# Kernel optimization log

Measured on AMD Instinct MI355X. Metric: run time of the kernel, lower is better.

## Reference

```python
import jax, jax.numpy as jnp
import numpy as np
from jax import lax

WINDOW_SIZE = 11
SIGMA = 1.5
MAX_VAL = 1.0
C1 = (MAX_VAL * 0.01) ** 2
C2 = (MAX_VAL * 0.03) ** 2


def _make_window(channel: int, k: int = WINDOW_SIZE, sigma: float = SIGMA) -> np.ndarray:
    x = np.arange(k, dtype=np.float64)
    g = np.exp(-((x - k // 2) ** 2) / (2.0 * sigma ** 2))
    g = (g / g.sum()).astype(np.float32)
    # rank-1 separable 3D window, built as dense [C,1,k,k,k] kernel (OIDHW, groups=C)
    w3 = g[:, None, None] * g[None, :, None] * g[None, None, :]
    return np.broadcast_to(w3, (channel, 1, k, k, k)).copy()


def _dwconv3d(x, kernel, pad):
    # depthwise 3D conv, SAME padding for odd kernel
    return lax.conv_general_dilated(
        x, kernel, window_strides=(1, 1, 1), padding=[(pad, pad)] * 3,
        dimension_numbers=("NCDHW", "OIDHW", "NCDHW"),
        feature_group_count=kernel.shape[0])


def setup_inputs() -> dict:
    key = jax.random.key(0)
    k1, k2 = jax.random.split(key)
    shape = (2, 4, 64, 160, 160)  # [B, C, D, H, W]
    img1 = jax.random.uniform(k1, shape, dtype=jnp.float32)
    img2 = jax.random.uniform(k2, shape, dtype=jnp.float32)
    return {"img1": img1, "img2": img2}


def reference(img1, img2):
    channel = img1.shape[1]
    window = jnp.asarray(_make_window(channel))
    pad = WINDOW_SIZE // 2
    # mask = ones_like(img1) in the original -> identity multiply, omitted
    mu1 = _dwconv3d(img1, window, pad)
    mu2 = _dwconv3d(img2, window, pad)
    mu1_sq = mu1 * mu1
    mu2_sq = mu2 * mu2
    mu1_mu2 = mu1 * mu2
    sigma1_sq = _dwconv3d(img1 * img1, window, pad) - mu1_sq
    sigma2_sq = _dwconv3d(img2 * img2, window, pad) - mu2_sq
    sigma12 = _dwconv3d(img1 * img2, window, pad) - mu1_mu2
    ssim_map = ((2.0 * mu1_mu2 + C1) * (2.0 * sigma12 + C2)) / (
        (mu1_sq + mu2_sq + C1) * (sigma1_sq + sigma2_sq + C2))
    ssim = jnp.mean(ssim_map, axis=(0, 2, 3, 4))  # per-channel SSIM, shape [C]
    return 1.0 - ssim
```

## Files before the change

### kernel.cpp

```cpp
#include <hip/hip_runtime.h>
#include <math.h>

typedef float v2f __attribute__((ext_vector_type(2)));

namespace {

constexpr int C_DIM = 4;
constexpr int D_DIM = 64;
constexpr int H_DIM = 160;
constexpr int W_DIM = 160;

constexpr int TH = 16;
constexpr int TW = 16;
constexpr int HALO = 5;
constexpr int EH = 26;
constexpr int EW = 26;
constexpr int XST = 27;
constexpr int MST = 17;
constexpr int NPIX = EH * EW;

constexpr int TILES_W = 10;
constexpr int TPC = 100;
constexpr int NBLOCKS = 2 * C_DIM * TPC;

constexpr float C1f = 1e-4f;
constexpr float C2f = 9e-4f;
constexpr float INV_N = 1.0f / (2.0f * 64.0f * 160.0f * 160.0f);

struct GW { float g[11]; };

}

__global__ void finalize_kernel(const float* __restrict__ partial,
                                float* __restrict__ out) {
    const int tid = threadIdx.x;
    const int c = tid >> 6;
    const int lane = tid & 63;
    float s = 0.0f;
#pragma unroll
    for (int b = 0; b < 2; ++b)
        for (int i = lane; i < TPC; i += 64)
            s += partial[b * (C_DIM * TPC) + c * TPC + i];
#pragma unroll
    for (int off = 32; off > 0; off >>= 1) s += __shfl_down(s, off, 64);
    if (lane == 0 && c < C_DIM) out[c] = 1.0f - s * INV_N;
}

__global__ __launch_bounds__(256, 4) void ssim3d_kernel(
    const float* __restrict__ img1, const float* __restrict__ img2,
    float* __restrict__ partial, GW gwp) {

    const int bid = blockIdx.x;
    const int tile = bid % TPC;
    const int c = (bid / TPC) % C_DIM;
    const int b = bid / (TPC * C_DIM);
    const int h0 = (tile / TILES_W) * TH;
    const int w0 = (tile % TILES_W) * TW;

    const long planeHW = (long)H_DIM * W_DIM;
    const long volbase = (long)(b * C_DIM + c) * D_DIM * planeHW;
    const long org = volbase + (long)(h0 - HALO) * W_DIM + (w0 - HALO);
    const float* __restrict__ p1 = img1 + org;
    const float* __restrict__ p2 = img2 + org;

    const bool interior = (h0 >= HALO) && (h0 + TH + HALO <= H_DIM) &&
                          (w0 >= HALO) && (w0 + TW + HALO <= W_DIM);

    __shared__ v2f    xy[2][EH][XST];
    __shared__ float4 mid[EH][MST];
    __shared__ float  rbuf[4];

    const int tid = threadIdx.x;

    int hh_[3], ww_[3], off_[3];
    bool live_[3], ok_[3];
#pragma unroll
    for (int k = 0; k < 3; ++k) {
        const int e = tid + k * 256;
        live_[k] = (e < NPIX);
        const int hh = e / EW;
        const int ww = e - hh * EW;
        hh_[k] = hh; ww_[k] = ww;
        off_[k] = hh * W_DIM + ww;
        const int gh = h0 - HALO + hh;
        const int gw = w0 - HALO + ww;
        ok_[k] = ((unsigned)gh < (unsigned)H_DIM) &&
                 ((unsigned)gw < (unsigned)W_DIM);
    }

    auto fetch_slice = [&](int s, v2f lv[3]) {
        const long sb = (long)s * planeHW;
#pragma unroll
        for (int k = 0; k < 3; ++k) {
            lv[k] = (v2f){0.0f, 0.0f};
            if (live_[k] && (interior || ok_[k])) {
                const long gi = sb + off_[k];
                lv[k].x = p1[gi];
                lv[k].y = p2[gi];
            }
        }
    };
    auto commit_slice = [&](int buf, const v2f lv[3]) {
#pragma unroll
        for (int k = 0; k < 3; ++k)
            if (live_[k]) xy[buf][hh_[k]][ww_[k]] = lv[k];
    };

    const bool wactive = (tid < 208);
    const int whh = tid % 26;
    const int wwg = (tid / 26) * 2;

    auto wconv = [&](int cur) {
        v2f a0 = {0.f, 0.f}, b0 = {0.f, 0.f};
        v2f a1 = {0.f, 0.f}, b1 = {0.f, 0.f};
#pragma unroll
        for (int t = 0; t < 12; ++t) {
            const v2f xv = xy[cur][whh][wwg + t];
            const v2f sq = xv * xv;
            v2f qp;
            qp.x = sq.x + sq.y;
            qp.y = xv.x * xv.y;
            if (t < 11) {
                const v2f g2 = {gwp.g[t], gwp.g[t]};
                a0 = __builtin_elementwise_fma(g2, xv, a0);
                b0 = __builtin_elementwise_fma(g2, qp, b0);
            }
            if (t >= 1) {
                const v2f g2 = {gwp.g[t - 1], gwp.g[t - 1]};
                a1 = __builtin_elementwise_fma(g2, xv, a1);
                b1 = __builtin_elementwise_fma(g2, qp, b1);
            }
        }
        mid[whh][wwg]     = make_float4(a0.x, a0.y, b0.x, b0.y);
        mid[whh][wwg + 1] = make_float4(a1.x, a1.y, b1.x, b1.y);
    };

    const int h_out = tid >> 4;
    const int w_out = tid & 15;
    v2f wxy[11], wqp[11];
#pragma unroll
    for (int i = 0; i < 11; ++i) {
        wxy[i] = (v2f){0.f, 0.f};
        wqp[i] = (v2f){0.f, 0.f};
    }
    float accum = 0.0f;

    auto hconv = [&](v2f& zxy, v2f& zqp) {
        zxy = (v2f){0.f, 0.f};
        zqp = (v2f){0.f, 0.f};
#pragma unroll
        for (int t = 0; t < 11; ++t) {
            const float4 m = mid[h_out + t][w_out];
            const v2f g2 = {gwp.g[t], gwp.g[t]};
            const v2f ma = {m.x, m.y};
            const v2f mb = {m.z, m.w};
            zxy = __builtin_elementwise_fma(g2, ma, zxy);
            zqp = __builtin_elementwise_fma(g2, mb, zqp);
        }
    };

    auto shift_insert = [&](v2f zxy, v2f zqp) {
#pragma unroll
        for (int i = 0; i < 10; ++i) {
            wxy[i] = wxy[i + 1];
            wqp[i] = wqp[i + 1];
        }
        wxy[10] = zxy;
        wqp[10] = zqp;
    };

    auto consume = [&]() {
        v2f mxy = {0.f, 0.f}, mqp = {0.f, 0.f};
#pragma unroll
        for (int t = 0; t < 11; ++t) {
            const v2f g2 = {gwp.g[t], gwp.g[t]};
            mxy = __builtin_elementwise_fma(g2, wxy[t], mxy);
            mqp = __builtin_elementwise_fma(g2, wqp[t], mqp);
        }
        const float m1 = mxy.x, m2 = mxy.y;
        const float q = mqp.x, pp = mqp.y;
        const float m1s = m1 * m1;
        const float m2s = m2 * m2;
        const float m12 = m1 * m2;
        const float spp = q - m1s - m2s;
        const float s12 = pp - m12;
        const float num = (2.0f * m12 + C1f) * (2.0f * s12 + C2f);
        const float den = (m1s + m2s + C1f) * (spp + C2f);
        accum = fmaf(num, __builtin_amdgcn_rcpf(den), accum);
    };

    {
        v2f lv[3];
        fetch_slice(0, lv);
        commit_slice(0, lv);
    }
    __syncthreads();

    for (int s = 0; s < D_DIM; ++s) {
        const int cur = s & 1;
        v2f lv[3];
        const bool have_next = (s + 1 < D_DIM);
        if (have_next) fetch_slice(s + 1, lv);
        if (wactive) wconv(cur);
        if (have_next) commit_slice(cur ^ 1, lv);
        __syncthreads();
        v2f zxy, zqp;
        hconv(zxy, zqp);
        shift_insert(zxy, zqp);
        if (s >= HALO) consume();
        __syncthreads();
    }
#pragma unroll
    for (int s = D_DIM; s < D_DIM + HALO; ++s) {
        shift_insert((v2f){0.f, 0.f}, (v2f){0.f, 0.f});
        consume();
    }

#pragma unroll
    for (int off = 32; off > 0; off >>= 1) accum += __shfl_down(accum, off, 64);
    const int wave = tid >> 6;
    const int lane = tid & 63;
    if (lane == 0) rbuf[wave] = accum;
    __syncthreads();
    if (tid == 0) partial[bid] = rbuf[0] + rbuf[1] + rbuf[2] + rbuf[3];
}

extern "C" void kernel_launch(void* const* d_in, const int* in_sizes, int n_in,
                              void* d_out, int out_size, void* d_ws, size_t ws_size,
                              hipStream_t stream) {
    const float* img1 = (const float*)d_in[0];
    const float* img2 = (const float*)d_in[1];
    float* out = (float*)d_out;
    float* partial = (float*)d_ws;

    GW gw;
    {
        double gd[11];
        double ssum = 0.0;
        for (int i = 0; i < 11; ++i) {
            const double t = (double)(i - 5);
            gd[i] = exp(-(t * t) / 4.5);
            ssum += gd[i];
        }
        for (int i = 0; i < 11; ++i) gw.g[i] = (float)(gd[i] / ssum);
    }

    ssim3d_kernel<<<NBLOCKS, 256, 0, stream>>>(img1, img2, partial, gw);
    finalize_kernel<<<1, 256, 0, stream>>>(partial, out);
}
```

Before: 230.2 us.

## Double-buffer mid tile to drop a barrier and unroll depth loop by four

Makes the intermediate mid buffer double-buffered so the second __syncthreads per depth slice can be removed, since wconv of the next slice now writes the other buffer. It also unrolls the depth loop by four and keeps a 14-entry register window, so the per-slice register shift is replaced by one shift every four slices. This halves barrier count and cuts register moves, at the cost of more shared memory and register pressure that may lower occupancy.

```diff
diff --git a/kernel.cpp b/kernel.cpp
--- a/kernel.cpp
+++ b/kernel.cpp
@@ -67,7 +67,7 @@
                           (w0 >= HALO) && (w0 + TW + HALO <= W_DIM);
 
     __shared__ v2f    xy[2][EH][XST];
-    __shared__ float4 mid[EH][MST];
+    __shared__ float4 mid[2][EH][MST];
     __shared__ float  rbuf[4];
 
     const int tid = threadIdx.x;
@@ -131,26 +131,18 @@
                 b1 = __builtin_elementwise_fma(g2, qp, b1);
             }
         }
-        mid[whh][wwg]     = make_float4(a0.x, a0.y, b0.x, b0.y);
-        mid[whh][wwg + 1] = make_float4(a1.x, a1.y, b1.x, b1.y);
+        mid[cur][whh][wwg]     = make_float4(a0.x, a0.y, b0.x, b0.y);
+        mid[cur][whh][wwg + 1] = make_float4(a1.x, a1.y, b1.x, b1.y);
     };
 
     const int h_out = tid >> 4;
     const int w_out = tid & 15;
-    v2f wxy[11], wqp[11];
-#pragma unroll
-    for (int i = 0; i < 11; ++i) {
-        wxy[i] = (v2f){0.f, 0.f};
-        wqp[i] = (v2f){0.f, 0.f};
-    }
-    float accum = 0.0f;
-
-    auto hconv = [&](v2f& zxy, v2f& zqp) {
+    auto hconv = [&](int cur, v2f& zxy, v2f& zqp) {
         zxy = (v2f){0.f, 0.f};
         zqp = (v2f){0.f, 0.f};
 #pragma unroll
         for (int t = 0; t < 11; ++t) {
-            const float4 m = mid[h_out + t][w_out];
+            const float4 m = mid[cur][h_out + t][w_out];
             const v2f g2 = {gwp.g[t], gwp.g[t]};
             const v2f ma = {m.x, m.y};
             const v2f mb = {m.z, m.w};
@@ -159,24 +151,8 @@
         }
     };
 
-    auto shift_insert = [&](v2f zxy, v2f zqp) {
-#pragma unroll
-        for (int i = 0; i < 10; ++i) {
-            wxy[i] = wxy[i + 1];
-            wqp[i] = wqp[i + 1];
-        }
-        wxy[10] = zxy;
-        wqp[10] = zqp;
-    };
-
-    auto consume = [&]() {
-        v2f mxy = {0.f, 0.f}, mqp = {0.f, 0.f};
-#pragma unroll
-        for (int t = 0; t < 11; ++t) {
-            const v2f g2 = {gwp.g[t], gwp.g[t]};
-            mxy = __builtin_elementwise_fma(g2, wxy[t], mxy);
-            mqp = __builtin_elementwise_fma(g2, wqp[t], mqp);
-        }
+    float accum = 0.0f;
+    auto ssim_add = [&](v2f mxy, v2f mqp) {
         const float m1 = mxy.x, m2 = mxy.y;
         const float q = mqp.x, pp = mqp.y;
         const float m1s = m1 * m1;
@@ -189,6 +165,13 @@
         accum = fmaf(num, __builtin_amdgcn_rcpf(den), accum);
     };
 
+    v2f wxy[14], wqp[14];
+#pragma unroll
+    for (int i = 0; i < 14; ++i) {
+        wxy[i] = (v2f){0.f, 0.f};
+        wqp[i] = (v2f){0.f, 0.f};
+    }
+
     {
         v2f lv[3];
         fetch_slice(0, lv);
@@ -196,24 +179,55 @@
     }
     __syncthreads();
 
-    for (int s = 0; s < D_DIM; ++s) {
-        const int cur = s & 1;
-        v2f lv[3];
-        const bool have_next = (s + 1 < D_DIM);
-        if (have_next) fetch_slice(s + 1, lv);
-        if (wactive) wconv(cur);
-        if (have_next) commit_slice(cur ^ 1, lv);
-        __syncthreads();
-        v2f zxy, zqp;
-        hconv(zxy, zqp);
-        shift_insert(zxy, zqp);
-        if (s >= HALO) consume();
-        __syncthreads();
-    }
-#pragma unroll
-    for (int s = D_DIM; s < D_DIM + HALO; ++s) {
-        shift_insert((v2f){0.f, 0.f}, (v2f){0.f, 0.f});
-        consume();
+    for (int sb = 0; sb < D_DIM; sb += 4) {
+#pragma unroll
+        for (int u = 0; u < 4; ++u) {
+            const int s = sb + u;
+            v2f lv[3];
+            const bool have_next = (s + 1 < D_DIM);
+            if (have_next) fetch_slice(s + 1, lv);
+            if (wactive) wconv(u & 1);
+            if (have_next) commit_slice((u + 1) & 1, lv);
+            __syncthreads();
+            v2f zxy, zqp;
+            hconv(u & 1, zxy, zqp);
+            wxy[10 + u] = zxy;
+            wqp[10 + u] = zqp;
+            if (s >= HALO) {
+                v2f mxy = {0.f, 0.f}, mqp = {0.f, 0.f};
+#pragma unroll
+                for (int t = 0; t < 11; ++t) {
+                    const v2f g2 = {gwp.g[t], gwp.g[t]};
+                    mxy = __builtin_elementwise_fma(g2, wxy[u + t], mxy);
+                    mqp = __builtin_elementwise_fma(g2, wqp[u + t], mqp);
+                }
+                ssim_add(mxy, mqp);
+            }
+        }
+#pragma unroll
+        for (int k = 0; k < 10; ++k) {
+            wxy[k] = wxy[k + 4];
+            wqp[k] = wqp[k + 4];
+        }
+    }
+
+#pragma unroll
+    for (int i = 10; i < 14; ++i) {
+        wxy[i] = (v2f){0.f, 0.f};
+        wqp[i] = (v2f){0.f, 0.f};
+    }
+#pragma unroll
+    for (int u2 = 0; u2 < 5; ++u2) {
+        v2f mxy = {0.f, 0.f}, mqp = {0.f, 0.f};
+#pragma unroll
+        for (int t = 0; t < 11; ++t) {
+            if (u2 + t <= 13) {
+                const v2f g2 = {gwp.g[t], gwp.g[t]};
+                mxy = __builtin_elementwise_fma(g2, wxy[u2 + t], mxy);
+                mqp = __builtin_elementwise_fma(g2, wqp[u2 + t], mqp);
+            }
+        }
+        ssim_add(mxy, mqp);
     }
 
 #pragma unroll
```

Measured after the change: 216.1 us. 1.07x faster.
